# Kernel optimization log

Hardware: AMD Instinct MI355X
Metric: run time of the kernel (lower is better)

The kernel has to match this reference:

```python
import jax, jax.numpy as jnp
import numpy as np

WINDOW = 2
OUT = 256


def setup_inputs() -> dict:
    key = jax.random.key(0)
    k1, k2 = jax.random.split(key)
    B, S, I = 8, 4096, 256
    x = jax.random.normal(k1, (B, S, I), dtype=jnp.float32)
    # fc: Linear(window*input -> 2*out*3)
    fan_in = WINDOW * I
    W_fc = jax.random.normal(k2, (2 * OUT * 3, fan_in), dtype=jnp.float32) / np.sqrt(fan_in)
    b_fc = jnp.zeros((2 * OUT * 3,), dtype=jnp.float32)
    return {"x": x, "W_fc": W_fc, "b_fc": b_fc}


def _forget_mult(z_t, f_t, reverse):
    # z_t, f_t: (S, B, O) time-major. c[t] = f[t]*c[prev] + (1-f[t])*z[t], c init 0.
    def step(c, fz):
        f, z = fz
        c = f * c + (1.0 - f) * z
        return c, c

    _, cs = jax.lax.scan(step, jnp.zeros_like(z_t[0]), (f_t, z_t), reverse=reverse)
    return cs  # (S, B, O)


def reference(x, W_fc, b_fc):
    B, S, I = x.shape
    pad = max(WINDOW - 1, 1)
    # stride(): left zero-pad then window of consecutive timesteps, flattened
    xp = jnp.pad(x, ((0, 0), (pad, 0), (0, 0)))
    win = jnp.concatenate([xp[:, k:k + S, :] for k in range(WINDOW)], axis=-1)  # (B,S,W*I)
    g = jnp.einsum('bsi,gi->bsg', win, W_fc) + b_fc  # (B,S,6*O)
    z, f, o = jnp.split(g, 3, axis=2)  # each (B,S,2*O)
    z = jnp.tanh(z)
    f = jax.nn.sigmoid(f)
    # time-major per-direction views
    zt = jnp.swapaxes(z.reshape(B, S, 2, OUT), 0, 1)  # (S,B,2,O)
    ft = jnp.swapaxes(f.reshape(B, S, 2, OUT), 0, 1)
    c_fwd = _forget_mult(zt[:, :, 0], ft[:, :, 0], reverse=False)
    c_bwd = _forget_mult(zt[:, :, 1], ft[:, :, 1], reverse=True)
    c = jnp.stack([c_fwd, c_bwd], axis=2)  # (S,B,2,O)
    c = jnp.swapaxes(c, 0, 1).reshape(B, S, 2 * OUT)
    return jax.nn.sigmoid(o) * c
```

## Files before the change

### kernel.cpp

```cpp
#include <hip/hip_runtime.h>
#include <hip/hip_bf16.h>
#include <stdint.h>

#define B_DIM 8
#define S_DIM 4096
#define I_DIM 256
#define M_DIM (B_DIM * S_DIM)
#define N_DIM 1536
#define K_DIM 512

#define TM 128
#define TN 128
#define BK 64
#define LT_STRIDE 136

#define NX4 ((M_DIM * I_DIM) / 4)
#define NW4 ((N_DIM * K_DIM) / 4)

typedef __attribute__((ext_vector_type(8))) short bf16x8;
typedef __attribute__((ext_vector_type(4))) float f32x4;
typedef _Float16 h2 __attribute__((ext_vector_type(2)));
typedef _Float16 h4 __attribute__((ext_vector_type(4)));
typedef _Float16 h8 __attribute__((ext_vector_type(8)));

typedef const void __attribute__((address_space(1)))* gas_ptr;
typedef void __attribute__((address_space(3)))* las_ptr;

__device__ __forceinline__ void gload_lds16(const void* g, void* l) {
    __builtin_amdgcn_global_load_lds((gas_ptr)(uintptr_t)g, (las_ptr)(uintptr_t)l, 16, 0, 0);
}

__device__ __forceinline__ float fast_sigmoid(float x) {
    return 1.0f / (1.0f + __expf(-x));
}
__device__ __forceinline__ float fast_tanh(float x) {
    float ax = fabsf(x);
    float e = __expf(-2.0f * ax);
    float t = (1.0f - e) / (1.0f + e);
    return copysignf(t, x);
}

__device__ __forceinline__ unsigned short f2bf(float f) {
    uint32_t u = __float_as_uint(f);
    uint32_t r = (u + 0x7FFFu + ((u >> 16) & 1u)) >> 16;
    return (unsigned short)r;
}

__global__ __launch_bounds__(256)
void cvt_all(const float* __restrict__ x, const float* __restrict__ W,
             unsigned short* __restrict__ xb, unsigned short* __restrict__ Wb,
             unsigned short* __restrict__ zp)
{
    int i = blockIdx.x * 256 + threadIdx.x;
    if (blockIdx.x == 0 && threadIdx.x < 64) zp[threadIdx.x] = 0;
    if (i < NX4) {
        float4 v = ((const float4*)x)[i];
        ushort4 o;
        o.x = f2bf(v.x); o.y = f2bf(v.y); o.z = f2bf(v.z); o.w = f2bf(v.w);
        ((ushort4*)xb)[i] = o;
    } else if (i < NX4 + NW4) {
        int j = i - NX4;
        float4 v = ((const float4*)W)[j];
        ushort4 o;
        o.x = f2bf(v.x); o.y = f2bf(v.y); o.z = f2bf(v.z); o.w = f2bf(v.w);
        ((ushort4*)Wb)[j] = o;
    }
}

__global__ __launch_bounds__(256, 2)
void qrnn_gemm(const __hip_bfloat16* __restrict__ x,
               const __hip_bfloat16* __restrict__ W,
               const float* __restrict__ bias,
               _Float16* __restrict__ gT,
               const __hip_bfloat16* __restrict__ zeroPage)
{
    __shared__ __hip_bfloat16 smem[TM * BK + TN * BK];
    __hip_bfloat16* lA = smem;
    __hip_bfloat16* lB = smem + TM * BK;
    _Float16* tsp = (_Float16*)smem;

    const int tid = threadIdx.x;
    const int w = tid >> 6;
    const int l = tid & 63;

    const int xcd  = blockIdx.x & 7;
    const int slot = blockIdx.x >> 3;
    const int tileN = slot % 12;
    const int tileM = xcd * 32 + slot / 12;
    const int m0 = tileM * TM;
    const int n0 = tileN * TN;
    const int bIdx = m0 >> 12;
    const int sBase = m0 & 4095;

    const int c8 = (l & 7) ^ ((l >> 3) & 7);
    const int rowInP = w * 8 + (l >> 3);

    const int la = l & 15, lq = l >> 4;
    const int wm = w >> 1, wn = w & 1;

    f32x4 acc[4][4] = {};

    for (int kt = 0; kt < K_DIM / BK; ++kt) {
        __syncthreads();
        const int kcol = kt * 64 + c8 * 8;
#pragma unroll
        for (int p = 0; p < 4; ++p) {
            const int r = p * 32 + rowInP;
            const int srow = sBase + r;
            const __hip_bfloat16* srcA;
            if (kcol < 256) {
                srcA = (srow == 0) ? zeroPage
                     : x + ((size_t)((bIdx << 12) + srow - 1) * 256 + kcol);
            } else {
                srcA = x + ((size_t)((bIdx << 12) + srow) * 256 + (kcol - 256));
            }
            gload_lds16(srcA, &lA[p * 2048 + w * 512]);
            gload_lds16(W + ((size_t)(n0 + r) * 512 + kcol), &lB[p * 2048 + w * 512]);
        }
        __syncthreads();

#pragma unroll
        for (int kk = 0; kk < 2; ++kk) {
            bf16x8 af[4], bfr[4];
#pragma unroll
            for (int i = 0; i < 4; ++i) {
                const int ra = wm * 64 + i * 16 + la;
                const int ch = (kk * 4 + lq) ^ (ra & 7);
                af[i] = *(const bf16x8*)&lA[ra * 64 + ch * 8];
            }
#pragma unroll
            for (int j = 0; j < 4; ++j) {
                const int rb = wn * 64 + j * 16 + la;
                const int ch = (kk * 4 + lq) ^ (rb & 7);
                bfr[j] = *(const bf16x8*)&lB[rb * 64 + ch * 8];
            }
#pragma unroll
            for (int i = 0; i < 4; ++i)
#pragma unroll
                for (int j = 0; j < 4; ++j)
                    acc[i][j] = __builtin_amdgcn_mfma_f32_16x16x32_bf16(
                        af[i], bfr[j], acc[i][j], 0, 0, 0);
        }
    }

    const int grp = tid >> 3;
    const int ln8 = tid & 7;
#pragma unroll
    for (int half = 0; half < 2; ++half) {
        __syncthreads();
        if (wn == half) {
#pragma unroll
            for (int j = 0; j < 4; ++j) {
                const int colL = j * 16 + la;
                const float bv = bias[n0 + half * 64 + colL];
                _Float16* base = tsp + colL * LT_STRIDE + wm * 64 + lq * 4;
#pragma unroll
                for (int i = 0; i < 4; ++i) {
                    h4 hv;
#pragma unroll
                    for (int rr = 0; rr < 4; ++rr)
                        hv[rr] = (_Float16)(acc[i][j][rr] + bv);
                    *(h4*)(base + i * 16) = hv;
                }
            }
        }
        __syncthreads();
#pragma unroll
        for (int it = 0; it < 4; ++it) {
            const int colL = grp + 32 * (it & 1);
            const int mseg = ln8 + 8 * (it >> 1);
            h8 v = *(const h8*)(tsp + colL * LT_STRIDE + mseg * 8);
            *(h8*)(gT + (size_t)(n0 + half * 64 + colL) * 32768 + m0 + mseg * 8) = v;
        }
    }
}

__global__ __launch_bounds__(256)
void qrnn_scan(const _Float16* __restrict__ gT, float* __restrict__ out)
{
    __shared__ _Float16 oc[16 * 512];

    const int wv = threadIdx.x >> 6;
    const int l  = threadIdx.x & 63;
    const int tc  = blockIdx.x & 7;
    const int cg  = (blockIdx.x >> 3) & 15;
    const int dir = (blockIdx.x >> 7) & 1;
    const int b   = blockIdx.x >> 8;
    const int t0  = tc * 512;

    const bool haveWarm = (dir == 0) ? (tc > 0) : (tc < 7);
    const int tw0 = (dir == 0) ? (t0 - 128) : (t0 + 512);

    h8 z8[4], f8[4], o8[4];
    h2 zw[4], fw[4];
#pragma unroll
    for (int cc = 0; cc < 4; ++cc) {
        const int oo = cg * 16 + wv * 4 + cc;
        const size_t colz = (size_t)(dir * 256 + oo) * 32768 + (b << 12);
        z8[cc] = *(const h8*)(gT + colz + t0 + l * 8);
        f8[cc] = *(const h8*)(gT + (size_t)512 * 32768 + colz + t0 + l * 8);
        o8[cc] = *(const h8*)(gT + (size_t)1024 * 32768 + colz + t0 + l * 8);
        if (haveWarm) {
            zw[cc] = *(const h2*)(gT + colz + tw0 + l * 2);
            fw[cc] = *(const h2*)(gT + (size_t)512 * 32768 + colz + tw0 + l * 2);
        }
    }

#pragma unroll
    for (int cc = 0; cc < 4; ++cc) {
        const int chl = wv * 4 + cc;

        float cinit = 0.0f;
        if (haveWarm) {
            float A = 1.0f, Bv = 0.0f;
            if (dir == 0) {
#pragma unroll
                for (int k = 0; k < 2; ++k) {
                    float f = fast_sigmoid((float)fw[cc][k]);
                    float g = (1.0f - f) * fast_tanh((float)zw[cc][k]);
                    Bv = f * Bv + g; A *= f;
                }
            } else {
#pragma unroll
                for (int k = 1; k >= 0; --k) {
                    float f = fast_sigmoid((float)fw[cc][k]);
                    float g = (1.0f - f) * fast_tanh((float)zw[cc][k]);
                    Bv = f * Bv + g; A *= f;
                }
            }
#pragma unroll
            for (int d = 1; d < 64; d <<= 1) {
                float Ao = __shfl_xor(A, d);
                float Bo = __shfl_xor(Bv, d);
                bool selfFirst = ((l & d) == 0);
                if (dir == 1) selfFirst = !selfFirst;
                if (selfFirst) { Bv = Ao * Bv + Bo; A = A * Ao; }
                else           { Bv = A * Bo + Bv; A = A * Ao; }
            }
            cinit = Bv;
        }

        float fa[8], ga[8];
        float A = 1.0f, Bv = 0.0f;
        if (dir == 0) {
#pragma unroll
            for (int k = 0; k < 8; ++k) {
                fa[k] = fast_sigmoid((float)f8[cc][k]);
                ga[k] = (1.0f - fa[k]) * fast_tanh((float)z8[cc][k]);
                Bv = fa[k] * Bv + ga[k]; A *= fa[k];
            }
        } else {
#pragma unroll
            for (int k = 7; k >= 0; --k) {
                fa[k] = fast_sigmoid((float)f8[cc][k]);
                ga[k] = (1.0f - fa[k]) * fast_tanh((float)z8[cc][k]);
                Bv = fa[k] * Bv + ga[k]; A *= fa[k];
            }
        }

        float Ae, Be;
        if (dir == 0) {
#pragma unroll
            for (int d = 1; d < 64; d <<= 1) {
                float Ao = __shfl_up(A, d);
                float Bo = __shfl_up(Bv, d);
                if (l >= d) { Bv = A * Bo + Bv; A = A * Ao; }
            }
            Ae = __shfl_up(A, 1); Be = __shfl_up(Bv, 1);
            if (l == 0) { Ae = 1.0f; Be = 0.0f; }
        } else {
#pragma unroll
            for (int d = 1; d < 64; d <<= 1) {
                float Ao = __shfl_down(A, d);
                float Bo = __shfl_down(Bv, d);
                if (l + d < 64) { Bv = A * Bo + Bv; A = A * Ao; }
            }
            Ae = __shfl_down(A, 1); Be = __shfl_down(Bv, 1);
            if (l == 63) { Ae = 1.0f; Be = 0.0f; }
        }

        float s = Ae * cinit + Be;
        h8 res;
        if (dir == 0) {
#pragma unroll
            for (int k = 0; k < 8; ++k) {
                s = fa[k] * s + ga[k];
                res[k] = (_Float16)(fast_sigmoid((float)o8[cc][k]) * s);
            }
        } else {
#pragma unroll
            for (int k = 7; k >= 0; --k) {
                s = fa[k] * s + ga[k];
                res[k] = (_Float16)(fast_sigmoid((float)o8[cc][k]) * s);
            }
        }
        *(h8*)&oc[chl * 512 + l * 8] = res;
    }
    __syncthreads();

    const int t2 = threadIdx.x * 2;
    float r0[16], r1[16];
#pragma unroll
    for (int ch = 0; ch < 16; ++ch) {
        h2 v = *(const h2*)&oc[ch * 512 + t2];
        r0[ch] = (float)v[0];
        r1[ch] = (float)v[1];
    }
    const size_t row0 = (size_t)((b << 12) + t0 + t2);
    float* po0 = out + row0 * 512 + dir * 256 + cg * 16;
    float* po1 = po0 + 512;
    *(float4*)(po0)      = make_float4(r0[0], r0[1], r0[2], r0[3]);
    *(float4*)(po0 + 4)  = make_float4(r0[4], r0[5], r0[6], r0[7]);
    *(float4*)(po0 + 8)  = make_float4(r0[8], r0[9], r0[10], r0[11]);
    *(float4*)(po0 + 12) = make_float4(r0[12], r0[13], r0[14], r0[15]);
    *(float4*)(po1)      = make_float4(r1[0], r1[1], r1[2], r1[3]);
    *(float4*)(po1 + 4)  = make_float4(r1[4], r1[5], r1[6], r1[7]);
    *(float4*)(po1 + 8)  = make_float4(r1[8], r1[9], r1[10], r1[11]);
    *(float4*)(po1 + 12) = make_float4(r1[12], r1[13], r1[14], r1[15]);
}

extern "C" void kernel_launch(void* const* d_in, const int* in_sizes, int n_in,
                              void* d_out, int out_size, void* d_ws, size_t ws_size,
                              hipStream_t stream)
{
    const float* x    = (const float*)d_in[0];
    const float* W    = (const float*)d_in[1];
    const float* bias = (const float*)d_in[2];
    float* out = (float*)d_out;

    char* ws = (char*)d_ws;
    size_t off = 0;
    __hip_bfloat16* xb = (__hip_bfloat16*)(ws + off); off += (size_t)M_DIM * I_DIM * 2;
    __hip_bfloat16* Wb = (__hip_bfloat16*)(ws + off); off += (size_t)N_DIM * K_DIM * 2;
    _Float16* gT = (_Float16*)(ws + off); off += (size_t)N_DIM * M_DIM * 2;
    unsigned short* zeroPage = (unsigned short*)(ws + off); off += 128;

    const int ncvt = NX4 + NW4;
    cvt_all<<<dim3((ncvt + 255) / 256), dim3(256), 0, stream>>>(
        x, W, (unsigned short*)xb, (unsigned short*)Wb, zeroPage);

    qrnn_gemm<<<dim3(256 * 12), dim3(256), 0, stream>>>(xb, Wb, bias, gT,
                                                        (const __hip_bfloat16*)zeroPage);

    qrnn_scan<<<dim3(B_DIM * 2 * 16 * 8), dim3(256), 0, stream>>>(gT, out);
}
```

Baseline: 196.8 us.

## Rewrite GEMM as 256x256 tile, 8-wave, double-buffered pipelined kernel

```diff
diff --git a/kernel.cpp b/kernel.cpp
--- a/kernel.cpp
+++ b/kernel.cpp
@@ -9,10 +9,9 @@
 #define N_DIM 1536
 #define K_DIM 512
 
-#define TM 128
-#define TN 128
-#define BK 64
-#define LT_STRIDE 136
+#define BM 256
+#define BN 256
+#define EP_STRIDE 264
 
 #define NX4 ((M_DIM * I_DIM) / 4)
 #define NW4 ((N_DIM * K_DIM) / 4)
@@ -67,95 +66,136 @@
     }
 }
 
-__global__ __launch_bounds__(256, 2)
+
+#define SBAR __builtin_amdgcn_s_barrier()
+#define LGK0 asm volatile("s_waitcnt lgkmcnt(0)" ::: "memory")
+#define FENCE asm volatile("" ::: "memory")
+
+#define STAGE_A(bufc, kt, half)                                               \
+    { _Pragma("unroll")                                                       \
+      for (int q = 0; q < 2; ++q) {                                           \
+          const int r_ = (half) * 128 + q * 64 + w8 + l3;                     \
+          const int srow_ = sBase + r_;                                       \
+          const __hip_bfloat16* src_;                                         \
+          if ((kt) < 4) {                                                     \
+              src_ = (srow_ == 0) ? zeroPage                                  \
+                   : x + ((size_t)((bIdx << 12) + srow_ - 1) * 256 + (kt) * 64 + csx); \
+          } else {                                                            \
+              src_ = x + ((size_t)((bIdx << 12) + srow_) * 256 + ((kt) - 4) * 64 + csx); \
+          }                                                                   \
+          gload_lds16(src_, &smem[(bufc) * 32768 + ((half) * 128 + q * 64 + w8) * 64]); \
+      } }
+
+#define STAGE_B(bufc, kt, half)                                               \
+    { _Pragma("unroll")                                                       \
+      for (int q = 0; q < 2; ++q) {                                           \
+          const int r_ = (half) * 128 + q * 64 + w8 + l3;                     \
+          gload_lds16(W + (size_t)(n0 + r_) * 512 + (kt) * 64 + csx,          \
+                      &smem[(bufc) * 32768 + 16384 + ((half) * 128 + q * 64 + w8) * 64]); \
+      } }
+
+#define PHASE_READS(bufc, kk, AF, BF)                                         \
+    { const int ch8_ = (((kk) * 4 + lq) ^ (la & 7)) * 8;                      \
+      _Pragma("unroll")                                                       \
+      for (int i = 0; i < 8; ++i)                                             \
+          AF[i] = *(const bf16x8*)&smem[(bufc) * 32768 + (wm * 128 + i * 16 + la) * 64 + ch8_]; \
+      _Pragma("unroll")                                                       \
+      for (int j = 0; j < 4; ++j)                                             \
+          BF[j] = *(const bf16x8*)&smem[(bufc) * 32768 + 16384 + (wn * 64 + j * 16 + la) * 64 + ch8_]; \
+    }
+
+#define MFMA16(AF, BF, IB)                                                    \
+    { __builtin_amdgcn_s_setprio(1);                                          \
+      _Pragma("unroll")                                                       \
+      for (int i = 0; i < 4; ++i)                                             \
+          _Pragma("unroll")                                                   \
+          for (int j = 0; j < 4; ++j)                                         \
+              acc[(IB) + i][j] = __builtin_amdgcn_mfma_f32_16x16x32_bf16(     \
+                  AF[(IB) + i], BF[j], acc[(IB) + i][j], 0, 0, 0);            \
+      __builtin_amdgcn_s_setprio(0); }
+
+#define TILE(bufc, stB, ktB, stA, ktA, VMW)                                   \
+    { bf16x8 a0[8], b0[4], a1[8], b1[4];                                      \
+                                                                      \
+      PHASE_READS(bufc, 0, a0, b0);                                           \
+      if (stB) STAGE_B((bufc) ^ 1, ktB, 0);                                   \
+      FENCE; SBAR; LGK0;                                                      \
+      MFMA16(a0, b0, 0);                                                      \
+      FENCE; SBAR;                                                            \
+                                                                      \
+      PHASE_READS(bufc, 1, a1, b1);                                           \
+      if (stB) STAGE_B((bufc) ^ 1, ktB, 1);                                   \
+      FENCE; SBAR; LGK0;                                                      \
+      MFMA16(a0, b0, 4);                                                      \
+      FENCE; SBAR;                                                            \
+                                                                      \
+      if (stA) STAGE_A(bufc, ktA, 0);                                         \
+      FENCE; SBAR;                                                            \
+      MFMA16(a1, b1, 0);                                                      \
+      FENCE; SBAR;                                                            \
+                                                                      \
+      if (stA) STAGE_A(bufc, ktA, 1);                                         \
+      FENCE; SBAR;                                                            \
+      MFMA16(a1, b1, 4);                                                      \
+      if ((VMW) == 4)      asm volatile("s_waitcnt vmcnt(4)" ::: "memory");   \
+      else if ((VMW) == 0) asm volatile("s_waitcnt vmcnt(0)" ::: "memory");   \
+      FENCE; SBAR; }
+
+__global__ __launch_bounds__(512, 2)
 void qrnn_gemm(const __hip_bfloat16* __restrict__ x,
                const __hip_bfloat16* __restrict__ W,
                const float* __restrict__ bias,
                _Float16* __restrict__ gT,
                const __hip_bfloat16* __restrict__ zeroPage)
 {
-    __shared__ __hip_bfloat16 smem[TM * BK + TN * BK];
-    __hip_bfloat16* lA = smem;
-    __hip_bfloat16* lB = smem + TM * BK;
-    _Float16* tsp = (_Float16*)smem;
+    __shared__ __hip_bfloat16 smem[65536];
 
     const int tid = threadIdx.x;
-    const int w = tid >> 6;
-    const int l = tid & 63;
+    const int wid = tid >> 6;
+    const int l   = tid & 63;
+    const int la = l & 15, lq = l >> 4;
+    const int wm = wid >> 2, wn = wid & 3;
+    const int w8 = wid * 8, l3 = l >> 3;
+    const int csx = ((l & 7) ^ l3) * 8;
 
     const int xcd  = blockIdx.x & 7;
     const int slot = blockIdx.x >> 3;
-    const int tileN = slot % 12;
-    const int tileM = xcd * 32 + slot / 12;
-    const int m0 = tileM * TM;
-    const int n0 = tileN * TN;
-    const int bIdx = m0 >> 12;
+    const int tileN = slot % 6;
+    const int tileM = xcd * 16 + slot / 6;
+    const int m0 = tileM * BM;
+    const int n0 = tileN * BN;
+    const int bIdx  = m0 >> 12;
     const int sBase = m0 & 4095;
 
-    const int c8 = (l & 7) ^ ((l >> 3) & 7);
-    const int rowInP = w * 8 + (l >> 3);
-
-    const int la = l & 15, lq = l >> 4;
-    const int wm = w >> 1, wn = w & 1;
-
-    f32x4 acc[4][4] = {};
-
-    for (int kt = 0; kt < K_DIM / BK; ++kt) {
-        __syncthreads();
-        const int kcol = kt * 64 + c8 * 8;
-#pragma unroll
-        for (int p = 0; p < 4; ++p) {
-            const int r = p * 32 + rowInP;
-            const int srow = sBase + r;
-            const __hip_bfloat16* srcA;
-            if (kcol < 256) {
-                srcA = (srow == 0) ? zeroPage
-                     : x + ((size_t)((bIdx << 12) + srow - 1) * 256 + kcol);
-            } else {
-                srcA = x + ((size_t)((bIdx << 12) + srow) * 256 + (kcol - 256));
-            }
-            gload_lds16(srcA, &lA[p * 2048 + w * 512]);
-            gload_lds16(W + ((size_t)(n0 + r) * 512 + kcol), &lB[p * 2048 + w * 512]);
-        }
-        __syncthreads();
-
-#pragma unroll
-        for (int kk = 0; kk < 2; ++kk) {
-            bf16x8 af[4], bfr[4];
-#pragma unroll
-            for (int i = 0; i < 4; ++i) {
-                const int ra = wm * 64 + i * 16 + la;
-                const int ch = (kk * 4 + lq) ^ (ra & 7);
-                af[i] = *(const bf16x8*)&lA[ra * 64 + ch * 8];
-            }
+    f32x4 acc[8][4] = {};
+
+    STAGE_A(0, 0, 0); STAGE_A(0, 0, 1);
+    STAGE_B(0, 0, 0); STAGE_B(0, 0, 1);
+    STAGE_A(1, 1, 0); STAGE_A(1, 1, 1);
+    asm volatile("s_waitcnt vmcnt(4)" ::: "memory");
+    SBAR;
+
+    for (int t2 = 0; t2 < 3; ++t2) {
+        const int kb = 2 * t2 + 1;
+        TILE(0, true, kb,     true, kb + 1, 4);
+        TILE(1, true, kb + 1, true, kb + 2, 4);
+    }
+    TILE(0, true, 7, false, 0, 0);
+    TILE(1, false, 0, false, 0, -1);
+    FENCE;
+
+    _Float16* tsp = (_Float16*)smem;
+#pragma unroll
+    for (int h = 0; h < 2; ++h) {
+        if (h) __syncthreads();
+        if ((wn >> 1) == h) {
 #pragma unroll
             for (int j = 0; j < 4; ++j) {
-                const int rb = wn * 64 + j * 16 + la;
-                const int ch = (kk * 4 + lq) ^ (rb & 7);
-                bfr[j] = *(const bf16x8*)&lB[rb * 64 + ch * 8];
-            }
-#pragma unroll
-            for (int i = 0; i < 4; ++i)
-#pragma unroll
-                for (int j = 0; j < 4; ++j)
-                    acc[i][j] = __builtin_amdgcn_mfma_f32_16x16x32_bf16(
-                        af[i], bfr[j], acc[i][j], 0, 0, 0);
-        }
-    }
-
-    const int grp = tid >> 3;
-    const int ln8 = tid & 7;
-#pragma unroll
-    for (int half = 0; half < 2; ++half) {
-        __syncthreads();
-        if (wn == half) {
-#pragma unroll
-            for (int j = 0; j < 4; ++j) {
-                const int colL = j * 16 + la;
-                const float bv = bias[n0 + half * 64 + colL];
-                _Float16* base = tsp + colL * LT_STRIDE + wm * 64 + lq * 4;
-#pragma unroll
-                for (int i = 0; i < 4; ++i) {
+                const int colL = (wn & 1) * 64 + j * 16 + la;
+                const float bv = bias[n0 + h * 128 + colL];
+                _Float16* base = tsp + colL * EP_STRIDE + wm * 128 + lq * 4;
+#pragma unroll
+                for (int i = 0; i < 8; ++i) {
                     h4 hv;
 #pragma unroll
                     for (int rr = 0; rr < 4; ++rr)
@@ -166,11 +206,11 @@
         }
         __syncthreads();
 #pragma unroll
-        for (int it = 0; it < 4; ++it) {
-            const int colL = grp + 32 * (it & 1);
-            const int mseg = ln8 + 8 * (it >> 1);
-            h8 v = *(const h8*)(tsp + colL * LT_STRIDE + mseg * 8);
-            *(h8*)(gT + (size_t)(n0 + half * 64 + colL) * 32768 + m0 + mseg * 8) = v;
+        for (int it = 0; it < 8; ++it) {
+            const int col = (tid >> 3) + 64 * (it & 1);
+            const int mch = (tid & 7) + 8 * (it >> 1);
+            h8 v = *(const h8*)(tsp + col * EP_STRIDE + mch * 8);
+            *(h8*)(gT + (size_t)(n0 + h * 128 + col) * 32768 + m0 + mch * 8) = v;
         }
     }
 }
@@ -339,8 +379,8 @@
     cvt_all<<<dim3((ncvt + 255) / 256), dim3(256), 0, stream>>>(
         x, W, (unsigned short*)xb, (unsigned short*)Wb, zeroPage);
 
-    qrnn_gemm<<<dim3(256 * 12), dim3(256), 0, stream>>>(xb, Wb, bias, gT,
-                                                        (const __hip_bfloat16*)zeroPage);
+    qrnn_gemm<<<dim3(768), dim3(512), 0, stream>>>(xb, Wb, bias, gT,
+                                                   (const __hip_bfloat16*)zeroPage);
 
     qrnn_scan<<<dim3(B_DIM * 2 * 16 * 8), dim3(256), 0, stream>>>(gT, out);
 }
```

After: 306.9 us. 1.56x slower.
